# Optimization experiments

Hardware: AMD Instinct MI355X
Metric: run time of the kernel (lower is better)

The kernel has to match this reference:

```python
import jax, jax.numpy as jnp
import numpy as np

B, T, V, E, H, N = 8, 128, 32000, 128, 256, 20
SHARPEN = 5.0
EPS = 1e-8  # torch cosine_similarity eps


def setup_inputs() -> dict:
    key = jax.random.key(0)
    ks = jax.random.split(key, 8)
    g = lambda k, shape, scale: (jax.random.normal(k, shape, dtype=jnp.float32) * scale)
    return {
        "x_ids": jax.random.randint(ks[0], (B, T), 0, V),
        "emb": g(ks[1], (V, E), 0.02),                 # nn.Embedding weight
        "W_i": g(ks[2], (H, E), E ** -0.5),            # rnn_i weight (no bias)
        "W_h": g(ks[3], (H, H), H ** -0.5),            # rnn_h weight
        "W_fc": g(ks[4], (V, 2 * H), (2 * H) ** -0.5), # fc -> vocab (softmaxed)
        "W_ops": g(ks[5], (3, 2 * H), (2 * H) ** -0.5),
        "W_choose": g(ks[6], (2, 2 * H), (2 * H) ** -0.5),
        "sharp": jnp.array([SHARPEN], dtype=jnp.float32),
    }


def _l2norm(x, eps=1e-12):
    # F.normalize(x, dim=-1)
    n = jnp.linalg.norm(x, axis=-1, keepdims=True)
    return x / jnp.maximum(n, eps)


def reference(x_ids, emb, W_i, W_h, W_fc, W_ops, W_choose, sharp):
    x = emb[x_ids]                                   # [B,T,E]
    # pre-normalize vocab rows for cosine-sim readout (clamped like torch)
    emb_cn = emb / jnp.maximum(jnp.linalg.norm(emb, axis=1, keepdims=True), EPS)
    sh = sharp[0]

    stack0 = jnp.full((B, N, E), 0.001, dtype=x.dtype)      # zero_offset + 0.001
    ptr0 = jnp.zeros((B, N), x.dtype).at[:, 0].set(1.0)     # pointer at slot 0
    h0 = jnp.zeros((B, H), x.dtype)

    def step(carry, xi):
        h, stack, ptr = carry
        ri = _l2norm(xi) @ W_i.T                     # rnn_i(normalize(x_t))
        h = jnp.tanh(ri + h @ W_h.T)
        hm = 1.0 - jax.nn.relu(h)
        hmod = jnp.concatenate([hm, hm], axis=1)     # [B,2H]
        # GumbelSoftmax(temp=1, hard=False) -> deterministic softmax (no noise)
        ops = jax.nn.softmax(hmod @ W_ops.T, axis=1)  # [B,3]
        push, pop, nop = ops[:, 0], ops[:, 1], ops[:, 2]
        # --- differentiable stack push/pop/nop ---
        pop_val = jnp.einsum('bn,bne->be', ptr, stack)      # soft read at pointer
        p_push = jnp.roll(ptr, 1, axis=1)
        p_pop = jnp.roll(ptr, -1, axis=1)
        new_ptr = push[:, None] * p_push + pop[:, None] * p_pop + nop[:, None] * ptr
        new_ptr = jnp.clip(new_ptr, EPS) ** sh              # sharpen
        new_ptr = new_ptr / jnp.sum(new_ptr, axis=1, keepdims=True)
        w = (push[:, None] * p_push)[:, :, None]            # write weight [B,N,1]
        new_stack = stack * (1.0 - w) + w * xi[:, None, :]
        # --- readout ---
        semantic = jax.nn.softmax(hmod @ W_fc.T, axis=1)    # [B,V]
        pv_n = pop_val / jnp.maximum(
            jnp.linalg.norm(pop_val, axis=1, keepdims=True), EPS)
        syntactic = pv_n @ emb_cn.T                          # cosine sim [B,V]
        choice = jax.nn.softmax(hmod @ W_choose.T, axis=1)   # [B,2]
        out = choice[:, 0:1] * semantic + choice[:, 1:2] * syntactic
        return (h, new_stack, new_ptr), out

    _, outs = jax.lax.scan(step, (h0, stack0, ptr0), jnp.swapaxes(x, 0, 1))
    return jnp.swapaxes(outs, 0, 1)  # [B,T,V]
```

## Files before the change

### kernel.cpp

```cpp
#include <hip/hip_runtime.h>
#include <hip/hip_bf16.h>
#include <stdint.h>

#define T_ 128
#define B_ 8
#define V_ 32000
#define E_ 128
#define H_ 256
#define N_ 20
#define M_ 1024
#define PIT 264
#define PIT2 136
#define NCH2 1000

typedef __attribute__((ext_vector_type(8))) short short8;
typedef __attribute__((ext_vector_type(4))) float f32x4;
typedef unsigned short ushort;

static __device__ __forceinline__ ushort f2bf_u(float f) {
  __hip_bfloat16 h = __float2bfloat16(f);
  return *reinterpret_cast<ushort*>(&h);
}

__global__ void whb_k(const float* __restrict__ Wh, uint4* __restrict__ whb4) {
  int idx = blockIdx.x*256 + threadIdx.x;
  int k8 = idx >> 8, i = idx & 255;
  const float* s = Wh + i*H_ + k8*8;
  uint4 o;
  o.x = (uint32_t)f2bf_u(s[0]) | ((uint32_t)f2bf_u(s[1]) << 16);
  o.y = (uint32_t)f2bf_u(s[2]) | ((uint32_t)f2bf_u(s[3]) << 16);
  o.z = (uint32_t)f2bf_u(s[4]) | ((uint32_t)f2bf_u(s[5]) << 16);
  o.w = (uint32_t)f2bf_u(s[6]) | ((uint32_t)f2bf_u(s[7]) << 16);
  whb4[idx] = o;
}

__global__ void wit_k(const float* __restrict__ Wi, float* __restrict__ WiT) {
  int idx = blockIdx.x*256 + threadIdx.x;
  if (idx < H_*E_) {
    int i = idx >> 7, e = idx & (E_-1);
    WiT[e*H_ + i] = Wi[idx];
  }
}

__global__ void embn_k(const float* __restrict__ emb, ushort* __restrict__ embnb) {
  int v = blockIdx.x, l = threadIdx.x;
  float e0 = emb[v*E_ + l];
  float e1 = emb[v*E_ + 64 + l];
  float ss = e0*e0 + e1*e1;
  #pragma unroll
  for (int off = 32; off >= 1; off >>= 1) ss += __shfl_xor(ss, off);
  float inv = 1.f / fmaxf(sqrtf(ss), 1e-8f);
  embnb[v*E_ + l]      = f2bf_u(e0*inv);
  embnb[v*E_ + 64 + l] = f2bf_u(e1*inv);
}

__global__ void foldfc_k(const float* __restrict__ Wfc, ushort* __restrict__ Wfcb) {
  int idx = blockIdx.x*256 + threadIdx.x;
  int n = idx >> 8, k = idx & 255;
  Wfcb[idx] = f2bf_u(Wfc[n*2*H_ + k] + Wfc[n*2*H_ + H_ + k]);
}

__global__ __launch_bounds__(256) void ri_k(const int* __restrict__ x_ids,
    const float* __restrict__ emb, const float* __restrict__ WiT,
    float* __restrict__ RI)
{
  __shared__ float xn[E_];
  __shared__ float red[2];
  int r = blockIdx.x, tid = threadIdx.x;
  int id = x_ids[r];
  float v = 0.f;
  if (tid < E_) v = emb[id*E_ + tid];
  float ss = v*v;
  if (tid < E_) {
    #pragma unroll
    for (int off = 32; off >= 1; off >>= 1) ss += __shfl_xor(ss, off);
    if ((tid & 63) == 0) red[tid >> 6] = ss;
  }
  __syncthreads();
  float inv = 1.f / fmaxf(sqrtf(red[0] + red[1]), 1e-12f);
  if (tid < E_) xn[tid] = v*inv;
  __syncthreads();
  float s = 0.f;
  for (int e = 0; e < E_; ++e) s += xn[e]*WiT[e*H_ + tid];
  RI[r*H_ + tid] = s;
}

__global__ __launch_bounds__(1024) void chain_k(
    const uint4* __restrict__ whb4, const float* __restrict__ RI,
    float* __restrict__ HMf, ushort* __restrict__ HMb)
{
  __shared__ uint4 wlds[32*256];
  __shared__ __align__(16) float hbuf[2][H_];
  __shared__ float hred[3][H_];
  const int b = blockIdx.x, tid = threadIdx.x;
  const int q = tid >> 8, i = tid & 255;

  for (int m = tid; m < 32*256; m += 1024) wlds[m] = whb4[m];
  if (q == 0) hbuf[0][i] = 0.f;
  __syncthreads();
  float ri_c = (q == 0) ? RI[(size_t)b*T_*H_ + i] : 0.f;

  for (int t = 0; t < T_; ++t) {
    const int r = b*T_ + t;
    float ri_n = 0.f;
    if (q == 0 && t+1 < T_) ri_n = RI[(size_t)(r+1)*H_ + i];
    const float4* h4 = reinterpret_cast<const float4*>(hbuf[t & 1]);
    float p0 = 0.f, p1 = 0.f, p2 = 0.f, p3 = 0.f;
    #pragma unroll
    for (int j = 0; j < 8; ++j) {
      uint4 w = wlds[(q*8 + j)*256 + i];
      float4 ha = h4[q*16 + 2*j];
      float4 hb = h4[q*16 + 2*j + 1];
      p0 += __uint_as_float(w.x << 16)*ha.x + __uint_as_float(w.x & 0xffff0000u)*ha.y;
      p1 += __uint_as_float(w.y << 16)*ha.z + __uint_as_float(w.y & 0xffff0000u)*ha.w;
      p2 += __uint_as_float(w.z << 16)*hb.x + __uint_as_float(w.z & 0xffff0000u)*hb.y;
      p3 += __uint_as_float(w.w << 16)*hb.z + __uint_as_float(w.w & 0xffff0000u)*hb.w;
    }
    float p = (p0 + p1) + (p2 + p3);
    if (q) hred[q-1][i] = p;
    __syncthreads();
    if (q == 0) {
      float s = ri_c + p + hred[0][i] + hred[1][i] + hred[2][i];
      float hn = tanhf(s);
      hbuf[(t+1) & 1][i] = hn;
      float hm = 1.f - fmaxf(hn, 0.f);
      HMf[(size_t)r*H_ + i] = hm;
      HMb[(size_t)r*H_ + i] = f2bf_u(hm);
    }
    ri_c = ri_n;
    __syncthreads();
  }
}

__global__ void pvn_k(const float* __restrict__ PV, ushort* __restrict__ PVNb) {
  int r = blockIdx.x, l = threadIdx.x;
  float a = PV[(size_t)r*E_ + l];
  float c = PV[(size_t)r*E_ + 64 + l];
  float ss = a*a + c*c;
  #pragma unroll
  for (int off = 32; off >= 1; off >>= 1) ss += __shfl_xor(ss, off);
  float inv = 1.f / fmaxf(sqrtf(ss), 1e-8f);
  PVNb[(size_t)r*E_ + l]      = f2bf_u(a*inv);
  PVNb[(size_t)r*E_ + 64 + l] = f2bf_u(c*inv);
}

__global__ __launch_bounds__(512) void stats3_k(const ushort* __restrict__ HMb,
    const ushort* __restrict__ Wfcb, const float* __restrict__ HMf,
    const float* __restrict__ W_ops, const float* __restrict__ W_ch,
    const float* __restrict__ sharp, const int* __restrict__ x_ids,
    const float* __restrict__ emb,
    float* __restrict__ SS, float* __restrict__ CH, float* __restrict__ PV)
{
  __shared__ __align__(16) ushort As[128*PIT];
  __shared__ __align__(16) ushort Bs[64*PIT];
  __shared__ float ops_l[T_*4];
  __shared__ float2 pw_l[T_*N_];
  __shared__ int ids_l[T_];
  const int tid = threadIdx.x;

  if (blockIdx.y == 8) {
    if (blockIdx.x >= B_) return;
    const int b = blockIdx.x;
    const int w = tid >> 6, l = tid & 63;
    float wo[5][4];
    #pragma unroll
    for (int k = 0; k < 3; ++k)
      #pragma unroll
      for (int j = 0; j < 4; ++j)
        wo[k][j] = W_ops[k*2*H_ + 4*l + j] + W_ops[k*2*H_ + H_ + 4*l + j];
    #pragma unroll
    for (int k = 0; k < 2; ++k)
      #pragma unroll
      for (int j = 0; j < 4; ++j)
        wo[3+k][j] = W_ch[k*2*H_ + 4*l + j] + W_ch[k*2*H_ + H_ + 4*l + j];
    if (tid < T_) ids_l[tid] = x_ids[b*T_ + tid];
    for (int rl = w*16; rl < w*16 + 16; ++rl) {
      int R = b*T_ + rl;
      float4 hm4 = reinterpret_cast<const float4*>(HMf + (size_t)R*H_)[l];
      float d0 = hm4.x*wo[0][0] + hm4.y*wo[0][1] + hm4.z*wo[0][2] + hm4.w*wo[0][3];
      float d1 = hm4.x*wo[1][0] + hm4.y*wo[1][1] + hm4.z*wo[1][2] + hm4.w*wo[1][3];
      float d2 = hm4.x*wo[2][0] + hm4.y*wo[2][1] + hm4.z*wo[2][2] + hm4.w*wo[2][3];
      float d3 = hm4.x*wo[3][0] + hm4.y*wo[3][1] + hm4.z*wo[3][2] + hm4.w*wo[3][3];
      float d4 = hm4.x*wo[4][0] + hm4.y*wo[4][1] + hm4.z*wo[4][2] + hm4.w*wo[4][3];
      #pragma unroll
      for (int off = 32; off >= 1; off >>= 1) {
        d0 += __shfl_xor(d0, off); d1 += __shfl_xor(d1, off); d2 += __shfl_xor(d2, off);
        d3 += __shfl_xor(d3, off); d4 += __shfl_xor(d4, off);
      }
      if (l == 0) {
        float mx = fmaxf(d0, fmaxf(d1, d2));
        float e0 = expf(d0-mx), e1 = expf(d1-mx), e2 = expf(d2-mx);
        float oi = 1.f/(e0+e1+e2);
        ops_l[rl*4+0] = e0*oi; ops_l[rl*4+1] = e1*oi; ops_l[rl*4+2] = e2*oi;
        float cm = fmaxf(d3, d4);
        float f0 = expf(d3-cm), f1 = expf(d4-cm);
        float ci = 1.f/(f0+f1);
        CH[R*2] = f0*ci; CH[R*2+1] = f1*ci;
      }
    }
    __syncthreads();
    if (tid < 64) {
      const float sh = sharp[0];
      float ptr = (tid == 0) ? 1.f : 0.f;
      const int lp = (tid + N_ - 1) % N_, ln = (tid + 1) % N_;
      for (int t = 0; t < T_; ++t) {
        float push = ops_l[t*4+0], pop = ops_l[t*4+1], nop = ops_l[t*4+2];
        float pp = __shfl(ptr, lp);
        float po = __shfl(ptr, ln);
        float wgt = push*pp;
        float raw = wgt + pop*po + nop*ptr;
        float np = 0.f;
        if (tid < N_) np = exp2f(sh * log2f(fmaxf(raw, 1e-8f)));
        float ssum = np;
        #pragma unroll
        for (int off = 1; off < 32; off <<= 1) ssum += __shfl_xor(ssum, off);
        if (tid < N_) {
          pw_l[t*N_ + tid] = make_float2(ptr, wgt);
          ptr = np / ssum;
        }
      }
    }
    __syncthreads();
    if (tid < E_) {
      const int e = tid;
      float stck[N_];
      #pragma unroll
      for (int n = 0; n < N_; ++n) stck[n] = 0.001f;
      float xi_c = emb[(size_t)ids_l[0]*E_ + e];
      for (int t = 0; t < T_; ++t) {
        float xi_n = (t+1 < T_) ? emb[(size_t)ids_l[t+1]*E_ + e] : 0.f;
        float pv = 0.f;
        #pragma unroll
        for (int n = 0; n < N_; ++n) {
          float2 pw = pw_l[t*N_ + n];
          pv += pw.x * stck[n];
          stck[n] += pw.y * (xi_c - stck[n]);
        }
        PV[(size_t)(b*T_ + t)*E_ + e] = pv;
        xi_c = xi_n;
      }
    }
    return;
  }

  const int Rb = blockIdx.y*128, Cb = blockIdx.x*64;
  {
    const uint4* srcA = (const uint4*)(HMb  + (size_t)Rb*H_);
    const uint4* srcB = (const uint4*)(Wfcb + (size_t)Cb*H_);
    #pragma unroll
    for (int it = 0; it < 8; ++it) {
      int idx = it*512 + tid, row = idx >> 5, c = idx & 31;
      *(uint4*)&As[row*PIT + c*8] = srcA[row*32 + c];
    }
    #pragma unroll
    for (int it = 0; it < 4; ++it) {
      int idx = it*512 + tid, row = idx >> 5, c = idx & 31;
      *(uint4*)&Bs[row*PIT + c*8] = srcB[row*32 + c];
    }
  }
  __syncthreads();
  const int wave = tid >> 6, lane = tid & 63;
  const int wr = wave >> 1, wc = wave & 1;
  const int lr = lane & 15, g = lane >> 4;
  f32x4 acc[2][2] = {};
  const ushort* Ab = &As[(wr*32 + lr)*PIT + g*8];
  const ushort* Bb = &Bs[(wc*32 + lr)*PIT + g*8];
  #pragma unroll
  for (int ks = 0; ks < 8; ++ks) {
    short8 a0 = *(const short8*)(Ab + ks*32);
    short8 a1 = *(const short8*)(Ab + 16*PIT + ks*32);
    short8 b0 = *(const short8*)(Bb + ks*32);
    short8 b1 = *(const short8*)(Bb + 16*PIT + ks*32);
    acc[0][0] = __builtin_amdgcn_mfma_f32_16x16x32_bf16(a0, b0, acc[0][0], 0, 0, 0);
    acc[0][1] = __builtin_amdgcn_mfma_f32_16x16x32_bf16(a0, b1, acc[0][1], 0, 0, 0);
    acc[1][0] = __builtin_amdgcn_mfma_f32_16x16x32_bf16(a1, b0, acc[1][0], 0, 0, 0);
    acc[1][1] = __builtin_amdgcn_mfma_f32_16x16x32_bf16(a1, b1, acc[1][1], 0, 0, 0);
  }
  const int chunk = blockIdx.x*2 + wc;
  #pragma unroll
  for (int mi = 0; mi < 2; ++mi)
    #pragma unroll
    for (int r = 0; r < 4; ++r) {
      float s = expf(acc[mi][0][r]) + expf(acc[mi][1][r]);
      #pragma unroll
      for (int off = 1; off < 16; off <<= 1) s += __shfl_xor(s, off);
      if (lr == 0) SS[(size_t)(Rb + wr*32 + mi*16 + g*4 + r)*NCH2 + chunk] = s;
    }
}

__global__ void reduce2_k(const float* __restrict__ SS, float* __restrict__ MS) {
  int row = blockIdx.x, l = threadIdx.x;
  float s = 0.f;
  for (int c = l; c < NCH2; c += 64) s += SS[(size_t)row*NCH2 + c];
  #pragma unroll
  for (int off = 32; off >= 1; off >>= 1) s += __shfl_xor(s, off);
  if (l == 0) MS[row] = 1.f/s;
}

__global__ __launch_bounds__(512) void final3_k(const ushort* __restrict__ HMb,
    const ushort* __restrict__ Wfcb, const ushort* __restrict__ PVNb,
    const ushort* __restrict__ embnb, const float* __restrict__ MS,
    const float* __restrict__ CH, float* __restrict__ out)
{
  __shared__ __align__(16) ushort As[128*PIT];
  __shared__ __align__(16) ushort Bs[64*PIT];
  const int tid = threadIdx.x;
  const int Rb = blockIdx.y*128, Cb = blockIdx.x*64;
  const int wave = tid >> 6, lane = tid & 63;
  const int wr = wave >> 1, wc = wave & 1;
  const int lr = lane & 15, g = lane >> 4;

  {
    const uint4* srcA = (const uint4*)(HMb  + (size_t)Rb*H_);
    const uint4* srcB = (const uint4*)(Wfcb + (size_t)Cb*H_);
    #pragma unroll
    for (int it = 0; it < 8; ++it) {
      int idx = it*512 + tid, row = idx >> 5, c = idx & 31;
      *(uint4*)&As[row*PIT + c*8] = srcA[row*32 + c];
    }
    #pragma unroll
    for (int it = 0; it < 4; ++it) {
      int idx = it*512 + tid, row = idx >> 5, c = idx & 31;
      *(uint4*)&Bs[row*PIT + c*8] = srcB[row*32 + c];
    }
  }
  __syncthreads();
  f32x4 accL[2][2] = {};
  {
    const ushort* Ab = &As[(wr*32 + lr)*PIT + g*8];
    const ushort* Bb = &Bs[(wc*32 + lr)*PIT + g*8];
    #pragma unroll
    for (int ks = 0; ks < 8; ++ks) {
      short8 a0 = *(const short8*)(Ab + ks*32);
      short8 a1 = *(const short8*)(Ab + 16*PIT + ks*32);
      short8 b0 = *(const short8*)(Bb + ks*32);
      short8 b1 = *(const short8*)(Bb + 16*PIT + ks*32);
      accL[0][0] = __builtin_amdgcn_mfma_f32_16x16x32_bf16(a0, b0, accL[0][0], 0, 0, 0);
      accL[0][1] = __builtin_amdgcn_mfma_f32_16x16x32_bf16(a0, b1, accL[0][1], 0, 0, 0);
      accL[1][0] = __builtin_amdgcn_mfma_f32_16x16x32_bf16(a1, b0, accL[1][0], 0, 0, 0);
      accL[1][1] = __builtin_amdgcn_mfma_f32_16x16x32_bf16(a1, b1, accL[1][1], 0, 0, 0);
    }
  }
  __syncthreads();
  {
    const uint4* srcA = (const uint4*)(PVNb  + (size_t)Rb*E_);
    const uint4* srcB = (const uint4*)(embnb + (size_t)Cb*E_);
    #pragma unroll
    for (int it = 0; it < 4; ++it) {
      int idx = it*512 + tid, row = idx >> 4, c = idx & 15;
      *(uint4*)&As[row*PIT2 + c*8] = srcA[row*16 + c];
    }
    #pragma unroll
    for (int it = 0; it < 2; ++it) {
      int idx = it*512 + tid, row = idx >> 4, c = idx & 15;
      *(uint4*)&Bs[row*PIT2 + c*8] = srcB[row*16 + c];
    }
  }
  __syncthreads();
  f32x4 accS[2][2] = {};
  {
    const ushort* Ab = &As[(wr*32 + lr)*PIT2 + g*8];
    const ushort* Bb = &Bs[(wc*32 + lr)*PIT2 + g*8];
    #pragma unroll
    for (int ks = 0; ks < 4; ++ks) {
      short8 a0 = *(const short8*)(Ab + ks*32);
      short8 a1 = *(const short8*)(Ab + 16*PIT2 + ks*32);
      short8 b0 = *(const short8*)(Bb + ks*32);
      short8 b1 = *(const short8*)(Bb + 16*PIT2 + ks*32);
      accS[0][0] = __builtin_amdgcn_mfma_f32_16x16x32_bf16(a0, b0, accS[0][0], 0, 0, 0);
      accS[0][1] = __builtin_amdgcn_mfma_f32_16x16x32_bf16(a0, b1, accS[0][1], 0, 0, 0);
      accS[1][0] = __builtin_amdgcn_mfma_f32_16x16x32_bf16(a1, b0, accS[1][0], 0, 0, 0);
      accS[1][1] = __builtin_amdgcn_mfma_f32_16x16x32_bf16(a1, b1, accS[1][1], 0, 0, 0);
    }
  }

  #pragma unroll
  for (int mi = 0; mi < 2; ++mi)
    #pragma unroll
    for (int r = 0; r < 4; ++r) {
      int row = Rb + wr*32 + mi*16 + g*4 + r;
      float Si = MS[row];
      float c0 = CH[row*2], c1 = CH[row*2+1];
      float v0 = c0*expf(accL[mi][0][r])*Si + c1*accS[mi][0][r];
      float v1 = c0*expf(accL[mi][1][r])*Si + c1*accS[mi][1][r];
      size_t base = (size_t)row*V_ + Cb + wc*32 + lr;
      out[base]      = v0;
      out[base + 16] = v1;
    }
}

extern "C" void kernel_launch(void* const* d_in, const int* in_sizes, int n_in,
                              void* d_out, int out_size, void* d_ws, size_t ws_size,
                              hipStream_t stream) {
  const int*   x_ids = (const int*)d_in[0];
  const float* emb   = (const float*)d_in[1];
  const float* W_i   = (const float*)d_in[2];
  const float* W_h   = (const float*)d_in[3];
  const float* W_fc  = (const float*)d_in[4];
  const float* W_ops = (const float*)d_in[5];
  const float* W_ch  = (const float*)d_in[6];
  const float* sharp = (const float*)d_in[7];
  float* out = (float*)d_out;

  float* ws    = (float*)d_ws;
  uint4*  whb4 = (uint4*)ws;
  float*  WiT  = ws + 65536;
  float*  RI   = WiT + 32768;
  float*  CH   = RI + 262144;
  float*  MS   = CH + 2048;
  float*  SS   = MS + 1024;
  float*  HMf  = SS + 1024000;
  float*  PV   = HMf + 262144;
  float*  fend = PV + 131072;
  ushort* HMb   = (ushort*)fend;
  ushort* PVNb  = HMb + 262144;
  ushort* Wfcb  = PVNb + 131072;
  ushort* embnb = Wfcb + 8192000;

  whb_k  <<<32, 256, 0, stream>>>(W_h, whb4);
  wit_k  <<<(H_*E_ + 255)/256, 256, 0, stream>>>(W_i, WiT);
  embn_k <<<V_, 64, 0, stream>>>(emb, embnb);
  foldfc_k<<<V_*H_/256, 256, 0, stream>>>(W_fc, Wfcb);
  ri_k   <<<M_, 256, 0, stream>>>(x_ids, emb, WiT, RI);
  chain_k<<<B_, 1024, 0, stream>>>(whb4, RI, HMf, HMb);
  stats3_k<<<dim3(V_/64, 9), 512, 0, stream>>>(HMb, Wfcb, HMf, W_ops, W_ch, sharp,
                                               x_ids, emb, SS, CH, PV);
  pvn_k  <<<M_, 64, 0, stream>>>(PV, PVNb);
  reduce2_k<<<M_, 64, 0, stream>>>(SS, MS);
  final3_k<<<dim3(V_/64, M_/128), 512, 0, stream>>>(HMb, Wfcb, PVNb, embnb, MS, CH, out);
}
```

Measured before the change: 443.0 us.

## Load A fragments straight to registers and shrink GEMM tiles to 32 columns

The stats and final GEMM kernels no longer stage the HM and PVN activation tiles in shared memory. Each wave loads its own 32 rows of A directly from global memory into registers, and only the Wfc and embedding B tiles go through LDS. Blocks drop to 256 threads and 32 vocab columns, which doubles the grid and cuts LDS per block, aiming at higher occupancy and fewer LDS round trips. The cost is more register pressure and A rows being re-read from global memory (or L2) by twice as many blocks.

```diff
diff --git a/kernel.cpp b/kernel.cpp
--- a/kernel.cpp
+++ b/kernel.cpp
@@ -144,22 +144,21 @@
   PVNb[(size_t)r*E_ + 64 + l] = f2bf_u(c*inv);
 }
 
-__global__ __launch_bounds__(512) void stats3_k(const ushort* __restrict__ HMb,
+__global__ __launch_bounds__(256) void stats4_k(const ushort* __restrict__ HMb,
     const ushort* __restrict__ Wfcb, const float* __restrict__ HMf,
     const float* __restrict__ W_ops, const float* __restrict__ W_ch,
     const float* __restrict__ sharp, const int* __restrict__ x_ids,
     const float* __restrict__ emb,
     float* __restrict__ SS, float* __restrict__ CH, float* __restrict__ PV)
 {
-  __shared__ __align__(16) ushort As[128*PIT];
-  __shared__ __align__(16) ushort Bs[64*PIT];
-  __shared__ float ops_l[T_*4];
-  __shared__ float2 pw_l[T_*N_];
-  __shared__ int ids_l[T_];
+  __shared__ __align__(16) char smem[23552];
   const int tid = threadIdx.x;
 
   if (blockIdx.y == 8) {
     if (blockIdx.x >= B_) return;
+    float*  ops_l = (float*)smem;
+    float2* pw_l  = (float2*)(smem + 2048);
+    int*    ids_l = (int*)(smem + 2048 + 20480);
     const int b = blockIdx.x;
     const int w = tid >> 6, l = tid & 63;
     float wo[5][4];
@@ -174,7 +173,7 @@
       for (int j = 0; j < 4; ++j)
         wo[3+k][j] = W_ch[k*2*H_ + 4*l + j] + W_ch[k*2*H_ + H_ + 4*l + j];
     if (tid < T_) ids_l[tid] = x_ids[b*T_ + tid];
-    for (int rl = w*16; rl < w*16 + 16; ++rl) {
+    for (int rl = w*32; rl < w*32 + 32; ++rl) {
       int R = b*T_ + rl;
       float4 hm4 = reinterpret_cast<const float4*>(HMf + (size_t)R*H_)[l];
       float d0 = hm4.x*wo[0][0] + hm4.y*wo[0][1] + hm4.z*wo[0][2] + hm4.w*wo[0][3];
@@ -243,40 +242,36 @@
     return;
   }
 
-  const int Rb = blockIdx.y*128, Cb = blockIdx.x*64;
+  ushort* Bs = (ushort*)smem;
+  const int Cb = blockIdx.x*32;
   {
-    const uint4* srcA = (const uint4*)(HMb  + (size_t)Rb*H_);
     const uint4* srcB = (const uint4*)(Wfcb + (size_t)Cb*H_);
     #pragma unroll
-    for (int it = 0; it < 8; ++it) {
-      int idx = it*512 + tid, row = idx >> 5, c = idx & 31;
-      *(uint4*)&As[row*PIT + c*8] = srcA[row*32 + c];
-    }
-    #pragma unroll
     for (int it = 0; it < 4; ++it) {
-      int idx = it*512 + tid, row = idx >> 5, c = idx & 31;
+      int idx = it*256 + tid, row = idx >> 5, c = idx & 31;
       *(uint4*)&Bs[row*PIT + c*8] = srcB[row*32 + c];
     }
   }
-  __syncthreads();
   const int wave = tid >> 6, lane = tid & 63;
-  const int wr = wave >> 1, wc = wave & 1;
   const int lr = lane & 15, g = lane >> 4;
+  const int Rw = blockIdx.y*128 + wave*32;
+  short8 a[2][8];
+  #pragma unroll
+  for (int m = 0; m < 2; ++m)
+    #pragma unroll
+    for (int ks = 0; ks < 8; ++ks)
+      a[m][ks] = *(const short8*)(HMb + (size_t)(Rw + m*16 + lr)*H_ + ks*32 + g*8);
+  __syncthreads();
   f32x4 acc[2][2] = {};
-  const ushort* Ab = &As[(wr*32 + lr)*PIT + g*8];
-  const ushort* Bb = &Bs[(wc*32 + lr)*PIT + g*8];
   #pragma unroll
   for (int ks = 0; ks < 8; ++ks) {
-    short8 a0 = *(const short8*)(Ab + ks*32);
-    short8 a1 = *(const short8*)(Ab + 16*PIT + ks*32);
-    short8 b0 = *(const short8*)(Bb + ks*32);
-    short8 b1 = *(const short8*)(Bb + 16*PIT + ks*32);
-    acc[0][0] = __builtin_amdgcn_mfma_f32_16x16x32_bf16(a0, b0, acc[0][0], 0, 0, 0);
-    acc[0][1] = __builtin_amdgcn_mfma_f32_16x16x32_bf16(a0, b1, acc[0][1], 0, 0, 0);
-    acc[1][0] = __builtin_amdgcn_mfma_f32_16x16x32_bf16(a1, b0, acc[1][0], 0, 0, 0);
-    acc[1][1] = __builtin_amdgcn_mfma_f32_16x16x32_bf16(a1, b1, acc[1][1], 0, 0, 0);
-  }
-  const int chunk = blockIdx.x*2 + wc;
+    short8 b0 = *(const short8*)(&Bs[lr*PIT + ks*32 + g*8]);
+    short8 b1 = *(const short8*)(&Bs[(16 + lr)*PIT + ks*32 + g*8]);
+    acc[0][0] = __builtin_amdgcn_mfma_f32_16x16x32_bf16(a[0][ks], b0, acc[0][0], 0, 0, 0);
+    acc[0][1] = __builtin_amdgcn_mfma_f32_16x16x32_bf16(a[0][ks], b1, acc[0][1], 0, 0, 0);
+    acc[1][0] = __builtin_amdgcn_mfma_f32_16x16x32_bf16(a[1][ks], b0, acc[1][0], 0, 0, 0);
+    acc[1][1] = __builtin_amdgcn_mfma_f32_16x16x32_bf16(a[1][ks], b1, acc[1][1], 0, 0, 0);
+  }
   #pragma unroll
   for (int mi = 0; mi < 2; ++mi)
     #pragma unroll
@@ -284,7 +279,7 @@
       float s = expf(acc[mi][0][r]) + expf(acc[mi][1][r]);
       #pragma unroll
       for (int off = 1; off < 16; off <<= 1) s += __shfl_xor(s, off);
-      if (lr == 0) SS[(size_t)(Rb + wr*32 + mi*16 + g*4 + r)*NCH2 + chunk] = s;
+      if (lr == 0) SS[(size_t)(Rw + mi*16 + g*4 + r)*NCH2 + blockIdx.x] = s;
     }
 }
 
@@ -297,93 +292,81 @@
   if (l == 0) MS[row] = 1.f/s;
 }
 
-__global__ __launch_bounds__(512) void final3_k(const ushort* __restrict__ HMb,
+__global__ __launch_bounds__(256) void final4_k(const ushort* __restrict__ HMb,
     const ushort* __restrict__ Wfcb, const ushort* __restrict__ PVNb,
     const ushort* __restrict__ embnb, const float* __restrict__ MS,
     const float* __restrict__ CH, float* __restrict__ out)
 {
-  __shared__ __align__(16) ushort As[128*PIT];
-  __shared__ __align__(16) ushort Bs[64*PIT];
+  __shared__ __align__(16) ushort Bs[32*PIT];
   const int tid = threadIdx.x;
-  const int Rb = blockIdx.y*128, Cb = blockIdx.x*64;
+  const int Cb = blockIdx.x*32;
   const int wave = tid >> 6, lane = tid & 63;
-  const int wr = wave >> 1, wc = wave & 1;
   const int lr = lane & 15, g = lane >> 4;
+  const int Rw = blockIdx.y*128 + wave*32;
 
   {
-    const uint4* srcA = (const uint4*)(HMb  + (size_t)Rb*H_);
     const uint4* srcB = (const uint4*)(Wfcb + (size_t)Cb*H_);
     #pragma unroll
-    for (int it = 0; it < 8; ++it) {
-      int idx = it*512 + tid, row = idx >> 5, c = idx & 31;
-      *(uint4*)&As[row*PIT + c*8] = srcA[row*32 + c];
-    }
-    #pragma unroll
     for (int it = 0; it < 4; ++it) {
-      int idx = it*512 + tid, row = idx >> 5, c = idx & 31;
+      int idx = it*256 + tid, row = idx >> 5, c = idx & 31;
       *(uint4*)&Bs[row*PIT + c*8] = srcB[row*32 + c];
     }
   }
+  short8 a[2][8];
+  #pragma unroll
+  for (int m = 0; m < 2; ++m)
+    #pragma unroll
+    for (int ks = 0; ks < 8; ++ks)
+      a[m][ks] = *(const short8*)(HMb + (size_t)(Rw + m*16 + lr)*H_ + ks*32 + g*8);
   __syncthreads();
   f32x4 accL[2][2] = {};
+  #pragma unroll
+  for (int ks = 0; ks < 8; ++ks) {
+    short8 b0 = *(const short8*)(&Bs[lr*PIT + ks*32 + g*8]);
+    short8 b1 = *(const short8*)(&Bs[(16 + lr)*PIT + ks*32 + g*8]);
+    accL[0][0] = __builtin_amdgcn_mfma_f32_16x16x32_bf16(a[0][ks], b0, accL[0][0], 0, 0, 0);
+    accL[0][1] = __builtin_amdgcn_mfma_f32_16x16x32_bf16(a[0][ks], b1, accL[0][1], 0, 0, 0);
+    accL[1][0] = __builtin_amdgcn_mfma_f32_16x16x32_bf16(a[1][ks], b0, accL[1][0], 0, 0, 0);
+    accL[1][1] = __builtin_amdgcn_mfma_f32_16x16x32_bf16(a[1][ks], b1, accL[1][1], 0, 0, 0);
+  }
+  __syncthreads();
+
   {
-    const ushort* Ab = &As[(wr*32 + lr)*PIT + g*8];
-    const ushort* Bb = &Bs[(wc*32 + lr)*PIT + g*8];
-    #pragma unroll
-    for (int ks = 0; ks < 8; ++ks) {
-      short8 a0 = *(const short8*)(Ab + ks*32);
-      short8 a1 = *(const short8*)(Ab + 16*PIT + ks*32);
-      short8 b0 = *(const short8*)(Bb + ks*32);
-      short8 b1 = *(const short8*)(Bb + 16*PIT + ks*32);
-      accL[0][0] = __builtin_amdgcn_mfma_f32_16x16x32_bf16(a0, b0, accL[0][0], 0, 0, 0);
-      accL[0][1] = __builtin_amdgcn_mfma_f32_16x16x32_bf16(a0, b1, accL[0][1], 0, 0, 0);
-      accL[1][0] = __builtin_amdgcn_mfma_f32_16x16x32_bf16(a1, b0, accL[1][0], 0, 0, 0);
-      accL[1][1] = __builtin_amdgcn_mfma_f32_16x16x32_bf16(a1, b1, accL[1][1], 0, 0, 0);
-    }
-  }
-  __syncthreads();
-  {
-    const uint4* srcA = (const uint4*)(PVNb  + (size_t)Rb*E_);
     const uint4* srcB = (const uint4*)(embnb + (size_t)Cb*E_);
     #pragma unroll
-    for (int it = 0; it < 4; ++it) {
-      int idx = it*512 + tid, row = idx >> 4, c = idx & 15;
-      *(uint4*)&As[row*PIT2 + c*8] = srcA[row*16 + c];
-    }
-    #pragma unroll
     for (int it = 0; it < 2; ++it) {
-      int idx = it*512 + tid, row = idx >> 4, c = idx & 15;
+      int idx = it*256 + tid, row = idx >> 4, c = idx & 15;
       *(uint4*)&Bs[row*PIT2 + c*8] = srcB[row*16 + c];
     }
   }
+  short8 a2[2][4];
+  #pragma unroll
+  for (int m = 0; m < 2; ++m)
+    #pragma unroll
+    for (int ks = 0; ks < 4; ++ks)
+      a2[m][ks] = *(const short8*)(PVNb + (size_t)(Rw + m*16 + lr)*E_ + ks*32 + g*8);
   __syncthreads();
   f32x4 accS[2][2] = {};
-  {
-    const ushort* Ab = &As[(wr*32 + lr)*PIT2 + g*8];
-    const ushort* Bb = &Bs[(wc*32 + lr)*PIT2 + g*8];
-    #pragma unroll
-    for (int ks = 0; ks < 4; ++ks) {
-      short8 a0 = *(const short8*)(Ab + ks*32);
-      short8 a1 = *(const short8*)(Ab + 16*PIT2 + ks*32);
-      short8 b0 = *(const short8*)(Bb + ks*32);
-      short8 b1 = *(const short8*)(Bb + 16*PIT2 + ks*32);
-      accS[0][0] = __builtin_amdgcn_mfma_f32_16x16x32_bf16(a0, b0, accS[0][0], 0, 0, 0);
-      accS[0][1] = __builtin_amdgcn_mfma_f32_16x16x32_bf16(a0, b1, accS[0][1], 0, 0, 0);
-      accS[1][0] = __builtin_amdgcn_mfma_f32_16x16x32_bf16(a1, b0, accS[1][0], 0, 0, 0);
-      accS[1][1] = __builtin_amdgcn_mfma_f32_16x16x32_bf16(a1, b1, accS[1][1], 0, 0, 0);
-    }
+  #pragma unroll
+  for (int ks = 0; ks < 4; ++ks) {
+    short8 b0 = *(const short8*)(&Bs[lr*PIT2 + ks*32 + g*8]);
+    short8 b1 = *(const short8*)(&Bs[(16 + lr)*PIT2 + ks*32 + g*8]);
+    accS[0][0] = __builtin_amdgcn_mfma_f32_16x16x32_bf16(a2[0][ks], b0, accS[0][0], 0, 0, 0);
+    accS[0][1] = __builtin_amdgcn_mfma_f32_16x16x32_bf16(a2[0][ks], b1, accS[0][1], 0, 0, 0);
+    accS[1][0] = __builtin_amdgcn_mfma_f32_16x16x32_bf16(a2[1][ks], b0, accS[1][0], 0, 0, 0);
+    accS[1][1] = __builtin_amdgcn_mfma_f32_16x16x32_bf16(a2[1][ks], b1, accS[1][1], 0, 0, 0);
   }
 
   #pragma unroll
   for (int mi = 0; mi < 2; ++mi)
     #pragma unroll
     for (int r = 0; r < 4; ++r) {
-      int row = Rb + wr*32 + mi*16 + g*4 + r;
+      int row = Rw + mi*16 + g*4 + r;
       float Si = MS[row];
       float c0 = CH[row*2], c1 = CH[row*2+1];
       float v0 = c0*expf(accL[mi][0][r])*Si + c1*accS[mi][0][r];
       float v1 = c0*expf(accL[mi][1][r])*Si + c1*accS[mi][1][r];
-      size_t base = (size_t)row*V_ + Cb + wc*32 + lr;
+      size_t base = (size_t)row*V_ + Cb + lr;
       out[base]      = v0;
       out[base + 16] = v1;
     }
@@ -423,9 +406,9 @@
   foldfc_k<<<V_*H_/256, 256, 0, stream>>>(W_fc, Wfcb);
   ri_k   <<<M_, 256, 0, stream>>>(x_ids, emb, WiT, RI);
   chain_k<<<B_, 1024, 0, stream>>>(whb4, RI, HMf, HMb);
-  stats3_k<<<dim3(V_/64, 9), 512, 0, stream>>>(HMb, Wfcb, HMf, W_ops, W_ch, sharp,
-                                               x_ids, emb, SS, CH, PV);
+  stats4_k<<<dim3(NCH2, 9), 256, 0, stream>>>(HMb, Wfcb, HMf, W_ops, W_ch, sharp,
+                                              x_ids, emb, SS, CH, PV);
   pvn_k  <<<M_, 64, 0, stream>>>(PV, PVNb);
   reduce2_k<<<M_, 64, 0, stream>>>(SS, MS);
-  final3_k<<<dim3(V_/64, M_/128), 512, 0, stream>>>(HMb, Wfcb, PVNb, embnb, MS, CH, out);
-}
+  final4_k<<<dim3(NCH2, M_/128), 256, 0, stream>>>(HMb, Wfcb, PVNb, embnb, MS, CH, out);
+}
```

After: 477.1 us. 7.7% more time.
